# Performance work log

Measured on AMD Instinct MI355X. Metric: run time of the kernel, lower is better.

## Reference

```python
import jax, jax.numpy as jnp
import numpy as np
from jax import lax

DIM = 256          # C
D_INNER = 512      # expand * dim
D_STATE = 16       # N
DT_RANK = 32       # ceil(d_inner / 16)
K_CONV = 4


def setup_inputs() -> dict:
    key = jax.random.key(0)
    ks = jax.random.split(key, 20)
    B, C, H, W = 2, DIM, 64, 64
    Di, N, R = D_INNER, D_STATE, DT_RANK
    s = 0.02
    inp = {
        "decoder_feat": jax.random.normal(ks[0], (B, C, H, W), jnp.float32),
        "encoder_feat": jax.random.normal(ks[1], (B, C, H, W), jnp.float32),
        # CrossMambaFusion params
        "dec_w": jax.random.normal(ks[2], (C, 2 * Di), jnp.float32) * s,
        "dec_b": jnp.zeros((2 * Di,), jnp.float32),
        "enc_w": jax.random.normal(ks[3], (C, Di), jnp.float32) * s,
        "enc_b": jnp.zeros((Di,), jnp.float32),
        "out_w": jax.random.normal(ks[4], (Di, C), jnp.float32) * s,
        "out_b": jnp.zeros((C,), jnp.float32),
        "ln_g": jnp.ones((C,), jnp.float32),
        "ln_b": jnp.zeros((C,), jnp.float32),
        # Mamba block params (inner dim = Di, expand=1.0)
        "in_w": jax.random.normal(ks[5], (Di, 2 * Di), jnp.float32) * s,
        "in_b": jnp.zeros((2 * Di,), jnp.float32),
        "conv_w": jax.random.normal(ks[6], (Di, 1, K_CONV), jnp.float32) * 0.1,
        "conv_b": jnp.zeros((Di,), jnp.float32),
        "x_proj_w": jax.random.normal(ks[7], (Di, R + 2 * N), jnp.float32) * s,
        "dt_w": jax.random.normal(ks[8], (R, Di), jnp.float32) * 0.1,
        "dt_b": jax.random.uniform(ks[9], (Di,), jnp.float32, -4.0, -2.0),  # small dt after softplus
        "A_log": jnp.log(jnp.tile(jnp.arange(1, N + 1, dtype=jnp.float32)[None, :], (Di, 1))),
        "D_param": jnp.ones((Di,), jnp.float32),
        "m_out_w": jax.random.normal(ks[10], (Di, Di), jnp.float32) * s,
        "m_out_b": jnp.zeros((Di,), jnp.float32),
    }
    return inp


def _mamba(x, in_w, in_b, conv_w, conv_b, x_proj_w, dt_w, dt_b, A_log, D_param, m_out_w, m_out_b):
    # x: (B, L, Di)
    Bsz, L, Di = x.shape
    N, R = D_STATE, DT_RANK
    xz = x @ in_w + in_b                      # (B, L, 2*Di)
    xm, z = jnp.split(xz, 2, axis=-1)
    # causal depthwise conv over the sequence axis
    xc = jnp.swapaxes(xm, 1, 2)               # (B, Di, L)
    xc = lax.conv_general_dilated(
        xc, conv_w, window_strides=(1,), padding=[(K_CONV - 1, 0)],
        dimension_numbers=("NCH", "OIH", "NCH"), feature_group_count=Di)
    xc = xc + conv_b[None, :, None]
    u = jax.nn.silu(jnp.swapaxes(xc, 1, 2))   # (B, L, Di)
    x_dbl = u @ x_proj_w                      # (B, L, R+2N)
    dt = jax.nn.softplus(x_dbl[..., :R] @ dt_w + dt_b)   # (B, L, Di)
    Bm = x_dbl[..., R:R + N]                  # (B, L, N)
    Cm = x_dbl[..., R + N:]                   # (B, L, N)
    A = -jnp.exp(A_log)                       # (Di, N)

    def step(h, t):
        dt_t, u_t, B_t, C_t = t               # (B,Di),(B,Di),(B,N),(B,N)
        dA = jnp.exp(dt_t[..., None] * A)     # (B, Di, N)
        h = h * dA + (dt_t * u_t)[..., None] * B_t[:, None, :]
        y = jnp.einsum("bdn,bn->bd", h, C_t)
        return h, y

    h0 = jnp.zeros((Bsz, Di, N), x.dtype)
    _, ys = lax.scan(step, h0, (jnp.swapaxes(dt, 0, 1), jnp.swapaxes(u, 0, 1),
                                jnp.swapaxes(Bm, 0, 1), jnp.swapaxes(Cm, 0, 1)))
    y = jnp.swapaxes(ys, 0, 1) + u * D_param  # skip connection via D
    y = y * jax.nn.silu(z)
    return y @ m_out_w + m_out_b


def reference(decoder_feat, encoder_feat, dec_w, dec_b, enc_w, enc_b, out_w, out_b,
              ln_g, ln_b, in_w, in_b, conv_w, conv_b, x_proj_w, dt_w, dt_b,
              A_log, D_param, m_out_w, m_out_b):
    B, C, H, W = decoder_feat.shape
    Di = D_INNER
    dec = jnp.transpose(decoder_feat, (0, 2, 3, 1)).reshape(B, H * W, C)
    enc = jnp.transpose(encoder_feat, (0, 2, 3, 1)).reshape(B, H * W, C)
    dec_proj = dec @ dec_w + dec_b
    dec_x, dec_gate = dec_proj[..., :Di], dec_proj[..., Di:]
    enc_p = enc @ enc_w + enc_b
    combined = dec_x * jax.nn.sigmoid(enc_p) + enc_p          # (B, L, Di)
    processed = _mamba(combined, in_w, in_b, conv_w, conv_b, x_proj_w,
                       dt_w, dt_b, A_log, D_param, m_out_w, m_out_b)
    out = (processed * jax.nn.sigmoid(dec_gate)) @ out_w + out_b
    res = out + dec
    mu = jnp.mean(res, axis=-1, keepdims=True)
    var = jnp.mean(jnp.square(res - mu), axis=-1, keepdims=True)
    res = (res - mu) * lax.rsqrt(var + 1e-5) * ln_g + ln_b
    return jnp.transpose(res.reshape(B, H, W, C), (0, 3, 1, 2))
```

## Files before the change

### kernel.cpp

```cpp
#include <hip/hip_runtime.h>
#include <hip/hip_bf16.h>

typedef __bf16 bf16x8_t __attribute__((ext_vector_type(8)));
typedef float f32x4_t __attribute__((ext_vector_type(4)));

__device__ __forceinline__ float sigmoidf_(float x) { return 1.0f / (1.0f + __expf(-x)); }
__device__ __forceinline__ float siluf_(float x) { return x * sigmoidf_(x); }
__device__ __forceinline__ float softplusf_(float x) {
    return fmaxf(x, 0.0f) + log1pf(__expf(-fabsf(x)));
}
__device__ __forceinline__ float b2f(ushort u) { return __uint_as_float(((unsigned)u) << 16); }
__device__ __forceinline__ ushort f2b(float f) {
    return (ushort)__bfloat16_as_ushort(__float2bfloat16(f));
}

__global__ __launch_bounds__(256) void k_prep(
    const float* __restrict__ dec_w, const float* __restrict__ enc_w,
    const float* __restrict__ in_w, const float* __restrict__ m_out_w,
    const float* __restrict__ out_w, const float* __restrict__ x_proj_w,
    const float* __restrict__ dt_w,
    const float* __restrict__ dec, const float* __restrict__ enc,
    __hip_bfloat16* __restrict__ dec_wT, __hip_bfloat16* __restrict__ enc_wT,
    __hip_bfloat16* __restrict__ in_wT, __hip_bfloat16* __restrict__ m_out_wT,
    __hip_bfloat16* __restrict__ out_wT, __hip_bfloat16* __restrict__ xpwT,
    __hip_bfloat16* __restrict__ dtwT,
    __hip_bfloat16* __restrict__ decL, __hip_bfloat16* __restrict__ encL)
{
    __shared__ float tile[64][65];
    if (blockIdx.x < 5312) {
        int gid = blockIdx.x * 256 + threadIdx.x;
        const float* src; __hip_bfloat16* dst; int lk, N, idx;
        if (gid < 262144)       { src = dec_w;    dst = dec_wT;   lk = 8; N = 1024; idx = gid; }
        else if (gid < 393216)  { src = enc_w;    dst = enc_wT;   lk = 8; N = 512;  idx = gid - 262144; }
        else if (gid < 917504)  { src = in_w;     dst = in_wT;    lk = 9; N = 1024; idx = gid - 393216; }
        else if (gid < 1179648) { src = m_out_w;  dst = m_out_wT; lk = 9; N = 512;  idx = gid - 917504; }
        else if (gid < 1310720) { src = out_w;    dst = out_wT;   lk = 9; N = 256;  idx = gid - 1179648; }
        else if (gid < 1343488) { src = x_proj_w; dst = xpwT;     lk = 9; N = 64;   idx = gid - 1310720; }
        else                    { src = dt_w;     dst = dtwT;     lk = 5; N = 512;  idx = gid - 1343488; }
        int K = 1 << lk;
        int n = idx >> lk, k = idx & (K - 1);
        dst[idx] = __float2bfloat16(src[(size_t)k * N + n]);
        return;
    }
    const int bid = blockIdx.x - 5312;
    const int t = threadIdx.x;
    const int ct = bid & 3;
    const int lt = (bid >> 2) & 63;
    const int sel = bid >> 8;
    const int b = sel & 1, ten = sel >> 1;
    const float* src = ten ? enc : dec;
    __hip_bfloat16* dst = ten ? encL : decL;
    const size_t ibase = (size_t)b * 256 * 4096 + (size_t)(ct * 64) * 4096 + (size_t)lt * 64;
#pragma unroll
    for (int i = 0; i < 16; ++i) {
        int c = i * 4 + (t >> 6), l = t & 63;
        tile[c][l] = src[ibase + (size_t)c * 4096 + l];
    }
    __syncthreads();
    const size_t obase = ((size_t)b * 4096 + (size_t)lt * 64) * 256 + ct * 64;
#pragma unroll
    for (int i = 0; i < 16; ++i) {
        int l = i * 4 + (t >> 6), c = t & 63;
        dst[obase + (size_t)l * 256 + c] = __float2bfloat16(tile[c][l]);
    }
}

template <int EPI, int K>
__global__ __launch_bounds__(256) void bgemm(
    const __hip_bfloat16* __restrict__ A, const __hip_bfloat16* __restrict__ Bt,
    const float* __restrict__ bias, void* __restrict__ out0,
    void* __restrict__ out1, const void* __restrict__ extra)
{
    __shared__ ushort At[128 * 32];
    __shared__ ushort Bl[128 * 32];
    const int tid = threadIdx.x;
    const int wave = tid >> 6, lane = tid & 63;
    const int n0 = blockIdx.x * 128, m0 = blockIdx.y * 128;
    const int wm = (wave >> 1) * 64, wn = (wave & 1) * 64;
    f32x4_t acc[4][4] = {};
    const int fr = lane & 15, fq = (lane >> 4) * 8;

    for (int k0 = 0; k0 < K; k0 += 32) {
#pragma unroll
        for (int q = 0; q < 2; ++q) {
            int idx = q * 256 + tid;
            int row = idx >> 2, ch = (idx & 3) * 8;
            uint4 va = *(const uint4*)&A[(size_t)(m0 + row) * K + k0 + ch];
            uint4 vb = *(const uint4*)&Bt[(size_t)(n0 + row) * K + k0 + ch];
            *(uint4*)&At[row * 32 + ch] = va;
            *(uint4*)&Bl[row * 32 + ch] = vb;
        }
        __syncthreads();
        bf16x8_t af[4], bf[4];
#pragma unroll
        for (int i = 0; i < 4; ++i) {
            af[i] = *(bf16x8_t*)&At[(wm + i * 16 + fr) * 32 + fq];
            bf[i] = *(bf16x8_t*)&Bl[(wn + i * 16 + fr) * 32 + fq];
        }
#pragma unroll
        for (int i = 0; i < 4; ++i)
#pragma unroll
            for (int j = 0; j < 4; ++j)
                acc[i][j] = __builtin_amdgcn_mfma_f32_16x16x32_bf16(af[i], bf[j], acc[i][j], 0, 0, 0);
        __syncthreads();
    }

    const int col = lane & 15, rbase = (lane >> 4) * 4;
#pragma unroll
    for (int i = 0; i < 4; ++i) {
#pragma unroll
        for (int j = 0; j < 4; ++j) {
#pragma unroll
            for (int r = 0; r < 4; ++r) {
                int m = m0 + wm + i * 16 + rbase + r;
                int n = n0 + wn + j * 16 + col;
                float v = acc[i][j][r] + bias[n];
                if (EPI == 0) {
                    ((__hip_bfloat16*)out0)[(size_t)m * 512 + n] = __float2bfloat16(v);
                } else if (EPI == 1) {
                    if (n < 512) {
                        float ep = __bfloat162float(((const __hip_bfloat16*)extra)[(size_t)m * 512 + n]);
                        ((__hip_bfloat16*)out0)[(size_t)m * 512 + n] =
                            __float2bfloat16(fmaf(v, sigmoidf_(ep), ep));
                    } else {
                        ((__hip_bfloat16*)out1)[(size_t)m * 512 + (n - 512)] =
                            __float2bfloat16(sigmoidf_(v));
                    }
                } else if (EPI == 2) {
                    if (n < 512)
                        ((__hip_bfloat16*)out0)[(size_t)m * 512 + n] = __float2bfloat16(v);
                    else
                        ((__hip_bfloat16*)out1)[(size_t)m * 512 + (n - 512)] =
                            __float2bfloat16(siluf_(v));
                } else {
                    float g = __bfloat162float(((const __hip_bfloat16*)extra)[(size_t)m * 512 + n]);
                    ((__hip_bfloat16*)out0)[(size_t)m * 512 + n] = __float2bfloat16(v * g);
                }
            }
        }
    }
}

#define CHUNK 16
#define NCHUNK 256

__global__ __launch_bounds__(512) void k_conv_scan(
    const __hip_bfloat16* __restrict__ xm, const float* __restrict__ conv_w,
    const float* __restrict__ conv_b, const __hip_bfloat16* __restrict__ xpwT,
    const __hip_bfloat16* __restrict__ dtwT, const float* __restrict__ dt_b,
    const float* __restrict__ A_log,
    __hip_bfloat16* __restrict__ u_out, float* __restrict__ Bm,
    float* __restrict__ Cm, __hip_bfloat16* __restrict__ dt_out,
    ushort* __restrict__ hpart, float* __restrict__ dtsums)
{
    __shared__ __align__(16) ushort us_dts[CHUNK][512 + 8];
    __shared__ __align__(16) ushort adt[CHUNK][32 + 8];
    __shared__ float BsL[CHUNK * 16];
    const int tid = threadIdx.x;
    const int wave = tid >> 6, lane = tid & 63;
    const int bl0 = blockIdx.x * CHUNK;
    const int l0 = bl0 & 4095;
    const int b = blockIdx.x >> 8;
    const int chunk = blockIdx.x & (NCHUNK - 1);
    const int fr = lane & 15, fq = (lane >> 4) * 8;
    const int col = lane & 15, rbase = (lane >> 4) * 4;

    float uarr[CHUNK];
    {
        const int d = tid;
        const float cw0 = conv_w[d * 4], cw1 = conv_w[d * 4 + 1];
        const float cw2 = conv_w[d * 4 + 2], cw3 = conv_w[d * 4 + 3];
        const float cb = conv_b[d];
        const ushort* xs = (const ushort*)xm;
        float x0 = (l0 >= 3) ? b2f(xs[(size_t)(bl0 - 3) * 512 + d]) : 0.f;
        float x1 = (l0 >= 2) ? b2f(xs[(size_t)(bl0 - 2) * 512 + d]) : 0.f;
        float x2 = (l0 >= 1) ? b2f(xs[(size_t)(bl0 - 1) * 512 + d]) : 0.f;
#pragma unroll
        for (int t = 0; t < CHUNK; ++t) {
            float x3 = b2f(xs[(size_t)(bl0 + t) * 512 + d]);
            float a = cb;
            a = fmaf(cw0, x0, a);
            a = fmaf(cw1, x1, a);
            a = fmaf(cw2, x2, a);
            a = fmaf(cw3, x3, a);
            float uv = siluf_(a);
            uarr[t] = uv;
            ushort ub = f2b(uv);
            us_dts[t][d] = ub;
            ((ushort*)u_out)[(size_t)(bl0 + t) * 512 + d] = ub;
            x0 = x1; x1 = x2; x2 = x3;
        }
    }
    __syncthreads();

    if (wave < 4) {
        const int n0w = wave * 16;
        f32x4_t acc = {};
        const __hip_bfloat16* bp = xpwT + (size_t)(n0w + fr) * 512;
#pragma unroll
        for (int k0 = 0; k0 < 512; k0 += 32) {
            bf16x8_t af = *(bf16x8_t*)&us_dts[fr][k0 + fq];
            bf16x8_t bf = *(const bf16x8_t*)&bp[k0 + fq];
            acc = __builtin_amdgcn_mfma_f32_16x16x32_bf16(af, bf, acc, 0, 0, 0);
        }
#pragma unroll
        for (int r = 0; r < 4; ++r) {
            int m = rbase + r;
            int n = n0w + col;
            float v = acc[r];
            if (n < 32) {
                adt[m][n] = f2b(v);
            } else if (n < 48) {
                BsL[m * 16 + (n - 32)] = v;
                Bm[(size_t)(bl0 + m) * 16 + (n - 32)] = v;
            } else {
                Cm[(size_t)(bl0 + m) * 16 + (n - 48)] = v;
            }
        }
    }
    __syncthreads();

    {
        bf16x8_t af = *(bf16x8_t*)&adt[fr][fq];
#pragma unroll
        for (int t = 0; t < 4; ++t) {
            int nt = wave * 4 + t;
            bf16x8_t bf = *(const bf16x8_t*)&dtwT[(size_t)(nt * 16 + fr) * 32 + fq];
            f32x4_t acc = {};
            acc = __builtin_amdgcn_mfma_f32_16x16x32_bf16(af, bf, acc, 0, 0, 0);
#pragma unroll
            for (int r = 0; r < 4; ++r) {
                int m = rbase + r;
                int n = nt * 16 + col;
                ushort dv = f2b(softplusf_(acc[r] + dt_b[n]));
                us_dts[m][n] = dv;
                ((ushort*)dt_out)[(size_t)(bl0 + m) * 512 + n] = dv;
            }
        }
    }
    __syncthreads();

    {
        const int d = tid;
        float Av[16];
#pragma unroll
        for (int n = 0; n < 16; n += 4) {
            float4 al = *(const float4*)&A_log[d * 16 + n];
            Av[n + 0] = -__expf(al.x);
            Av[n + 1] = -__expf(al.y);
            Av[n + 2] = -__expf(al.z);
            Av[n + 3] = -__expf(al.w);
        }
        float h[16] = {};
        float dtsum = 0.f;
#pragma unroll
        for (int t = 0; t < CHUNK; ++t) {
            float dtv = b2f(us_dts[t][d]);
            float dtu = dtv * uarr[t];
            dtsum += dtv;
            const float* Bt = &BsL[t * 16];
#pragma unroll
            for (int n = 0; n < 16; ++n)
                h[n] = fmaf(h[n], __expf(dtv * Av[n]), dtu * Bt[n]);
        }
        const size_t sidx = ((size_t)b * NCHUNK + chunk) * 512 + d;
        const size_t idx = sidx * 16;
        ushort hb[16];
#pragma unroll
        for (int n = 0; n < 16; ++n) hb[n] = f2b(h[n]);
        *(uint4*)&hpart[idx]     = *(uint4*)&hb[0];
        *(uint4*)&hpart[idx + 8] = *(uint4*)&hb[8];
        dtsums[sidx] = dtsum;
    }
}

__global__ __launch_bounds__(64) void k_scan_comb(
    const ushort* __restrict__ hpart, const float* __restrict__ dtsums,
    const float* __restrict__ A_log, ushort* __restrict__ h_in)
{
    const int gid = blockIdx.x * 64 + threadIdx.x;
    const int n = gid & 15;
    const int d = (gid >> 4) & 511;
    const int b = gid >> 13;
    const float Av = -__expf(A_log[d * 16 + n]);
    float h = 0.f;
    for (int c = 0; c < NCHUNK; ++c) {
        const size_t sidx = ((size_t)b * NCHUNK + c) * 512 + d;
        const size_t idx = sidx * 16 + n;
        h_in[idx] = f2b(h);
        h = fmaf(h, __expf(Av * dtsums[sidx]), b2f(hpart[idx]));
    }
}

__global__ __launch_bounds__(512) void k_scan_fin(
    const __hip_bfloat16* __restrict__ dt, const __hip_bfloat16* __restrict__ u,
    const float* __restrict__ Bmp, const float* __restrict__ Cmp,
    const float* __restrict__ A_log, const float* __restrict__ Dp,
    const __hip_bfloat16* __restrict__ zs, const ushort* __restrict__ h_in,
    __hip_bfloat16* __restrict__ yout)
{
    __shared__ float Bs[CHUNK * 16];
    __shared__ float Cs[CHUNK * 16];
    const int d = threadIdx.x;
    const int chunk = blockIdx.x & (NCHUNK - 1);
    const int b = blockIdx.x >> 8;
    const size_t row0 = (size_t)b * 4096 + (size_t)chunk * CHUNK;

    if (d < CHUNK * 16) {
        Bs[d] = Bmp[row0 * 16 + d];
        Cs[d] = Cmp[row0 * 16 + d];
    }
    float Av[16];
#pragma unroll
    for (int n = 0; n < 16; n += 4) {
        float4 al = *(const float4*)&A_log[d * 16 + n];
        Av[n + 0] = -__expf(al.x);
        Av[n + 1] = -__expf(al.y);
        Av[n + 2] = -__expf(al.z);
        Av[n + 3] = -__expf(al.w);
    }
    const float Dv = Dp[d];
    float h[16];
    {
        const size_t idx = (((size_t)b * NCHUNK + chunk) * 512 + d) * 16;
        ushort hb[16];
        *(uint4*)&hb[0] = *(const uint4*)&h_in[idx];
        *(uint4*)&hb[8] = *(const uint4*)&h_in[idx + 8];
#pragma unroll
        for (int n = 0; n < 16; ++n) h[n] = b2f(hb[n]);
    }
    __syncthreads();

    const ushort* dtp = (const ushort*)dt + row0 * 512 + d;
    const ushort* up = (const ushort*)u + row0 * 512 + d;
    const ushort* zp = (const ushort*)zs + row0 * 512 + d;
    __hip_bfloat16* yp = yout + row0 * 512 + d;
#pragma unroll
    for (int t = 0; t < CHUNK; ++t) {
        float dtv = b2f(dtp[(size_t)t * 512]);
        float uv = b2f(up[(size_t)t * 512]);
        float zv = b2f(zp[(size_t)t * 512]);
        float dtu = dtv * uv;
        const float* Bt = &Bs[t * 16];
        const float* Ct = &Cs[t * 16];
        float y = 0.f;
#pragma unroll
        for (int n = 0; n < 16; ++n) {
            h[n] = fmaf(h[n], __expf(dtv * Av[n]), dtu * Bt[n]);
            y = fmaf(h[n], Ct[n], y);
        }
        yp[(size_t)t * 512] = __float2bfloat16((y + uv * Dv) * zv);
    }
}

__global__ __launch_bounds__(256) void k_out_ln(
    const __hip_bfloat16* __restrict__ A, const __hip_bfloat16* __restrict__ Bt,
    const float* __restrict__ bias, const __hip_bfloat16* __restrict__ decL,
    const float* __restrict__ ln_g, const float* __restrict__ ln_b,
    float* __restrict__ outp)
{
    __shared__ ushort At[32 * 32];
    __shared__ ushort Bl[256 * 32];
    __shared__ float red[4][32][2];
    __shared__ float lmu[32], lsc[32];
    const int tid = threadIdx.x;
    const int wave = tid >> 6, lane = tid & 63;
    const int m0 = blockIdx.x * 32;
    const int wn = wave * 64;
    f32x4_t acc[2][4] = {};
    const int fr = lane & 15, fq = (lane >> 4) * 8;

    for (int k0 = 0; k0 < 512; k0 += 32) {
        if (tid < 128) {
            int row = tid >> 2, ch = (tid & 3) * 8;
            *(uint4*)&At[row * 32 + ch] = *(const uint4*)&A[(size_t)(m0 + row) * 512 + k0 + ch];
        }
#pragma unroll
        for (int q = 0; q < 4; ++q) {
            int idx = q * 256 + tid;
            int row = idx >> 2, ch = (idx & 3) * 8;
            *(uint4*)&Bl[row * 32 + ch] = *(const uint4*)&Bt[(size_t)row * 512 + k0 + ch];
        }
        __syncthreads();
        bf16x8_t af[2], bf[4];
#pragma unroll
        for (int i = 0; i < 2; ++i)
            af[i] = *(bf16x8_t*)&At[(i * 16 + fr) * 32 + fq];
#pragma unroll
        for (int j = 0; j < 4; ++j)
            bf[j] = *(bf16x8_t*)&Bl[(wn + j * 16 + fr) * 32 + fq];
#pragma unroll
        for (int i = 0; i < 2; ++i)
#pragma unroll
            for (int j = 0; j < 4; ++j)
                acc[i][j] = __builtin_amdgcn_mfma_f32_16x16x32_bf16(af[i], bf[j], acc[i][j], 0, 0, 0);
        __syncthreads();
    }

    const int col = lane & 15, rbase = (lane >> 4) * 4;
#pragma unroll
    for (int i = 0; i < 2; ++i) {
#pragma unroll
        for (int r = 0; r < 4; ++r) {
            int ml = i * 16 + rbase + r;
            int m = m0 + ml;
            float s = 0.f, sq = 0.f;
#pragma unroll
            for (int j = 0; j < 4; ++j) {
                int n = wn + j * 16 + col;
                float dv = b2f(((const ushort*)decL)[(size_t)m * 256 + n]);
                float v = acc[i][j][r] + bias[n] + dv;
                acc[i][j][r] = v;
                s += v;
                sq = fmaf(v, v, sq);
            }
            s += __shfl_xor(s, 1);  sq += __shfl_xor(sq, 1);
            s += __shfl_xor(s, 2);  sq += __shfl_xor(sq, 2);
            s += __shfl_xor(s, 4);  sq += __shfl_xor(sq, 4);
            s += __shfl_xor(s, 8);  sq += __shfl_xor(sq, 8);
            if (col == 0) { red[wave][ml][0] = s; red[wave][ml][1] = sq; }
        }
    }
    __syncthreads();
    if (tid < 32) {
        float s  = red[0][tid][0] + red[1][tid][0] + red[2][tid][0] + red[3][tid][0];
        float sq = red[0][tid][1] + red[1][tid][1] + red[2][tid][1] + red[3][tid][1];
        float mu = s * (1.0f / 256.0f);
        float var = sq * (1.0f / 256.0f) - mu * mu;
        lmu[tid] = mu;
        lsc[tid] = rsqrtf(var + 1e-5f);
    }
    __syncthreads();
    const int bb = m0 >> 12;
    const int lpos0 = m0 & 4095;
#pragma unroll
    for (int i = 0; i < 2; ++i) {
#pragma unroll
        for (int r = 0; r < 4; ++r) {
            int ml = i * 16 + rbase + r;
            float mu = lmu[ml], sc = lsc[ml];
#pragma unroll
            for (int j = 0; j < 4; ++j) {
                int n = wn + j * 16 + col;
                float v = (acc[i][j][r] - mu) * sc * ln_g[n] + ln_b[n];
                outp[(size_t)bb * (256 * 4096) + (size_t)n * 4096 + lpos0 + ml] = v;
            }
        }
    }
}

extern "C" void kernel_launch(void* const* d_in, const int* in_sizes, int n_in,
                              void* d_out, int out_size, void* d_ws, size_t ws_size,
                              hipStream_t stream)
{
    const float* decoder_feat = (const float*)d_in[0];
    const float* encoder_feat = (const float*)d_in[1];
    const float* dec_w = (const float*)d_in[2];
    const float* dec_b = (const float*)d_in[3];
    const float* enc_w = (const float*)d_in[4];
    const float* enc_b = (const float*)d_in[5];
    const float* out_w = (const float*)d_in[6];
    const float* out_b = (const float*)d_in[7];
    const float* ln_g = (const float*)d_in[8];
    const float* ln_bb = (const float*)d_in[9];
    const float* in_w = (const float*)d_in[10];
    const float* in_b = (const float*)d_in[11];
    const float* conv_w = (const float*)d_in[12];
    const float* conv_b = (const float*)d_in[13];
    const float* x_proj_w = (const float*)d_in[14];
    const float* dt_w = (const float*)d_in[15];
    const float* dt_b = (const float*)d_in[16];
    const float* A_log = (const float*)d_in[17];
    const float* D_param = (const float*)d_in[18];
    const float* m_out_w = (const float*)d_in[19];
    const float* m_out_b = (const float*)d_in[20];

    float* outp = (float*)d_out;
    char* ws = (char*)d_ws;
    const size_t MB = 1024ull * 1024;
    __hip_bfloat16* decL     = (__hip_bfloat16*)(ws + 0 * MB);
    __hip_bfloat16* encL     = (__hip_bfloat16*)(ws + 4 * MB);
    __hip_bfloat16* dec_wT   = (__hip_bfloat16*)(ws + 8 * MB);
    __hip_bfloat16* enc_wT   = (__hip_bfloat16*)(ws + 9 * MB);
    __hip_bfloat16* in_wT    = (__hip_bfloat16*)(ws + 10 * MB);
    __hip_bfloat16* m_out_wT = (__hip_bfloat16*)(ws + 11 * MB);
    __hip_bfloat16* out_wT   = (__hip_bfloat16*)(ws + 12 * MB);
    __hip_bfloat16* xpwT     = (__hip_bfloat16*)(ws + 12 * MB + 262144);
    __hip_bfloat16* dtwT     = (__hip_bfloat16*)(ws + 12 * MB + 262144 + 65536);
    __hip_bfloat16* enc_pb   = (__hip_bfloat16*)(ws + 13 * MB);
    __hip_bfloat16* combined = (__hip_bfloat16*)(ws + 29 * MB);
    __hip_bfloat16* gate_sig = (__hip_bfloat16*)(ws + 37 * MB);
    __hip_bfloat16* xm       = (__hip_bfloat16*)(ws + 45 * MB);
    __hip_bfloat16* z_silu   = (__hip_bfloat16*)(ws + 53 * MB);
    __hip_bfloat16* u_buf    = (__hip_bfloat16*)(ws + 61 * MB);
    __hip_bfloat16* dt_buf   = (__hip_bfloat16*)(ws + 69 * MB);
    ushort* h_in             = (ushort*)(ws + 77 * MB);
    float* Bm                = (float*)(ws + 93 * MB);
    float* Cm                = (float*)(ws + 93 * MB + 524288);
    float* dtsums            = (float*)(ws + 94 * MB);
    ushort* hpart = (ushort*)(ws + 13 * MB);
    __hip_bfloat16* y_buf = combined;
    __hip_bfloat16* gated = xm;

    k_prep<<<6336, 256, 0, stream>>>(
        dec_w, enc_w, in_w, m_out_w, out_w, x_proj_w, dt_w,
        decoder_feat, encoder_feat,
        dec_wT, enc_wT, in_wT, m_out_wT, out_wT, xpwT, dtwT, decL, encL);
    bgemm<0, 256><<<dim3(4, 64), 256, 0, stream>>>(
        encL, enc_wT, enc_b, enc_pb, nullptr, nullptr);
    bgemm<1, 256><<<dim3(8, 64), 256, 0, stream>>>(
        decL, dec_wT, dec_b, combined, gate_sig, enc_pb);
    bgemm<2, 512><<<dim3(8, 64), 256, 0, stream>>>(
        combined, in_wT, in_b, xm, z_silu, nullptr);
    k_conv_scan<<<2 * NCHUNK, 512, 0, stream>>>(
        xm, conv_w, conv_b, xpwT, dtwT, dt_b, A_log,
        u_buf, Bm, Cm, dt_buf, hpart, dtsums);
    k_scan_comb<<<256, 64, 0, stream>>>(hpart, dtsums, A_log, h_in);
    k_scan_fin<<<2 * NCHUNK, 512, 0, stream>>>(
        dt_buf, u_buf, Bm, Cm, A_log, D_param, z_silu, h_in, y_buf);
    bgemm<3, 512><<<dim3(4, 64), 256, 0, stream>>>(
        y_buf, m_out_wT, m_out_b, gated, nullptr, gate_sig);
    k_out_ln<<<256, 256, 0, stream>>>(
        gated, out_wT, out_b, decL, ln_g, ln_bb, outp);
}
```

Baseline: 283.7 us.

## Fuse Mamba output projection, gating, out-projection and LayerNorm into one tail kernel

Replaces the separate m_out GEMM (with sigmoid-gate epilogue) and the out-projection+LayerNorm kernel with a single 512-thread kernel. Each block keeps its 32 rows in LDS, computes the first GEMM, writes the gated bf16 result back into the LDS tile, then runs the second GEMM and LayerNorm. Weight B operands are read directly from global memory instead of being staged through LDS. The NCHW output store is transposed through LDS so that each thread writes contiguous runs. This removes one launch and the round trip of the gated intermediate through global memory. In exchange, every block reads both full weight matrices from global/L2 with no LDS reuse.

```diff
diff --git a/kernel.cpp b/kernel.cpp
--- a/kernel.cpp
+++ b/kernel.cpp
@@ -126,15 +126,12 @@
                         ((__hip_bfloat16*)out1)[(size_t)m * 512 + (n - 512)] =
                             __float2bfloat16(sigmoidf_(v));
                     }
-                } else if (EPI == 2) {
+                } else {
                     if (n < 512)
                         ((__hip_bfloat16*)out0)[(size_t)m * 512 + n] = __float2bfloat16(v);
                     else
                         ((__hip_bfloat16*)out1)[(size_t)m * 512 + (n - 512)] =
                             __float2bfloat16(siluf_(v));
-                } else {
-                    float g = __bfloat162float(((const __hip_bfloat16*)extra)[(size_t)m * 512 + n]);
-                    ((__hip_bfloat16*)out0)[(size_t)m * 512 + n] = __float2bfloat16(v * g);
                 }
             }
         }
@@ -353,73 +350,99 @@
     }
 }
 
-__global__ __launch_bounds__(256) void k_out_ln(
-    const __hip_bfloat16* __restrict__ A, const __hip_bfloat16* __restrict__ Bt,
-    const float* __restrict__ bias, const __hip_bfloat16* __restrict__ decL,
+__global__ __launch_bounds__(512) void k_tail(
+    const __hip_bfloat16* __restrict__ y, const __hip_bfloat16* __restrict__ m_out_wT,
+    const float* __restrict__ m_out_b, const __hip_bfloat16* __restrict__ gate_sig,
+    const __hip_bfloat16* __restrict__ out_wT, const float* __restrict__ out_b,
+    const __hip_bfloat16* __restrict__ decL,
     const float* __restrict__ ln_g, const float* __restrict__ ln_b,
     float* __restrict__ outp)
 {
-    __shared__ ushort At[32 * 32];
-    __shared__ ushort Bl[256 * 32];
-    __shared__ float red[4][32][2];
-    __shared__ float lmu[32], lsc[32];
+    __shared__ __align__(16) char smem[32 * 520 * 2 + 1024 + 256];
+    ushort (*tile)[520] = (ushort(*)[520])smem;
+    float (*lt)[257] = (float(*)[257])smem;
+    float (*red)[32][2] = (float(*)[32][2])(smem + 33280);
+    float* lmu = (float*)(smem + 33280 + 1024);
+    float* lsc = lmu + 32;
+
     const int tid = threadIdx.x;
     const int wave = tid >> 6, lane = tid & 63;
     const int m0 = blockIdx.x * 32;
-    const int wn = wave * 64;
-    f32x4_t acc[2][4] = {};
     const int fr = lane & 15, fq = (lane >> 4) * 8;
-
+    const int col = lane & 15, rbase = (lane >> 4) * 4;
+
+    {
+        int row = tid >> 4, ch = (tid & 15) * 32;
+        const ushort* src = (const ushort*)y + (size_t)(m0 + row) * 512 + ch;
+#pragma unroll
+        for (int q = 0; q < 4; ++q)
+            *(uint4*)&tile[row][ch + q * 8] = *(const uint4*)&src[q * 8];
+    }
+    __syncthreads();
+
+    const int wn1 = wave * 64;
+    f32x4_t acc1[2][4] = {};
+#pragma unroll
     for (int k0 = 0; k0 < 512; k0 += 32) {
-        if (tid < 128) {
-            int row = tid >> 2, ch = (tid & 3) * 8;
-            *(uint4*)&At[row * 32 + ch] = *(const uint4*)&A[(size_t)(m0 + row) * 512 + k0 + ch];
-        }
-#pragma unroll
-        for (int q = 0; q < 4; ++q) {
-            int idx = q * 256 + tid;
-            int row = idx >> 2, ch = (idx & 3) * 8;
-            *(uint4*)&Bl[row * 32 + ch] = *(const uint4*)&Bt[(size_t)row * 512 + k0 + ch];
-        }
-        __syncthreads();
         bf16x8_t af[2], bf[4];
 #pragma unroll
         for (int i = 0; i < 2; ++i)
-            af[i] = *(bf16x8_t*)&At[(i * 16 + fr) * 32 + fq];
+            af[i] = *(bf16x8_t*)&tile[i * 16 + fr][k0 + fq];
 #pragma unroll
         for (int j = 0; j < 4; ++j)
-            bf[j] = *(bf16x8_t*)&Bl[(wn + j * 16 + fr) * 32 + fq];
+            bf[j] = *(const bf16x8_t*)&m_out_wT[(size_t)(wn1 + j * 16 + fr) * 512 + k0 + fq];
 #pragma unroll
         for (int i = 0; i < 2; ++i)
 #pragma unroll
             for (int j = 0; j < 4; ++j)
-                acc[i][j] = __builtin_amdgcn_mfma_f32_16x16x32_bf16(af[i], bf[j], acc[i][j], 0, 0, 0);
-        __syncthreads();
-    }
-
-    const int col = lane & 15, rbase = (lane >> 4) * 4;
-#pragma unroll
-    for (int i = 0; i < 2; ++i) {
-#pragma unroll
-        for (int r = 0; r < 4; ++r) {
-            int ml = i * 16 + rbase + r;
-            int m = m0 + ml;
-            float s = 0.f, sq = 0.f;
-#pragma unroll
-            for (int j = 0; j < 4; ++j) {
-                int n = wn + j * 16 + col;
-                float dv = b2f(((const ushort*)decL)[(size_t)m * 256 + n]);
-                float v = acc[i][j][r] + bias[n] + dv;
-                acc[i][j][r] = v;
-                s += v;
-                sq = fmaf(v, v, sq);
+                acc1[i][j] = __builtin_amdgcn_mfma_f32_16x16x32_bf16(af[i], bf[j], acc1[i][j], 0, 0, 0);
+    }
+    __syncthreads();
+
+#pragma unroll
+    for (int i = 0; i < 2; ++i)
+#pragma unroll
+        for (int j = 0; j < 4; ++j)
+#pragma unroll
+            for (int r = 0; r < 4; ++r) {
+                int ml = i * 16 + rbase + r;
+                int n = wn1 + j * 16 + col;
+                float g = b2f(((const ushort*)gate_sig)[(size_t)(m0 + ml) * 512 + n]);
+                tile[ml][n] = f2b((acc1[i][j][r] + m_out_b[n]) * g);
             }
-            s += __shfl_xor(s, 1);  sq += __shfl_xor(sq, 1);
-            s += __shfl_xor(s, 2);  sq += __shfl_xor(sq, 2);
-            s += __shfl_xor(s, 4);  sq += __shfl_xor(sq, 4);
-            s += __shfl_xor(s, 8);  sq += __shfl_xor(sq, 8);
-            if (col == 0) { red[wave][ml][0] = s; red[wave][ml][1] = sq; }
-        }
+    __syncthreads();
+
+    const int mh = wave >> 2, wn2 = (wave & 3) * 64;
+    f32x4_t acc2[4] = {};
+#pragma unroll
+    for (int k0 = 0; k0 < 512; k0 += 32) {
+        bf16x8_t af = *(bf16x8_t*)&tile[mh * 16 + fr][k0 + fq];
+#pragma unroll
+        for (int j = 0; j < 4; ++j) {
+            bf16x8_t bf = *(const bf16x8_t*)&out_wT[(size_t)(wn2 + j * 16 + fr) * 512 + k0 + fq];
+            acc2[j] = __builtin_amdgcn_mfma_f32_16x16x32_bf16(af, bf, acc2[j], 0, 0, 0);
+        }
+    }
+
+#pragma unroll
+    for (int r = 0; r < 4; ++r) {
+        int ml = mh * 16 + rbase + r;
+        int m = m0 + ml;
+        float s = 0.f, sq = 0.f;
+#pragma unroll
+        for (int j = 0; j < 4; ++j) {
+            int n = wn2 + j * 16 + col;
+            float dv = b2f(((const ushort*)decL)[(size_t)m * 256 + n]);
+            float v = acc2[j][r] + out_b[n] + dv;
+            acc2[j][r] = v;
+            s += v;
+            sq = fmaf(v, v, sq);
+        }
+        s += __shfl_xor(s, 1);  sq += __shfl_xor(sq, 1);
+        s += __shfl_xor(s, 2);  sq += __shfl_xor(sq, 2);
+        s += __shfl_xor(s, 4);  sq += __shfl_xor(sq, 4);
+        s += __shfl_xor(s, 8);  sq += __shfl_xor(sq, 8);
+        if (col == 0) { red[wave & 3][ml][0] = s; red[wave & 3][ml][1] = sq; }
     }
     __syncthreads();
     if (tid < 32) {
@@ -431,21 +454,27 @@
         lsc[tid] = rsqrtf(var + 1e-5f);
     }
     __syncthreads();
-    const int bb = m0 >> 12;
-    const int lpos0 = m0 & 4095;
-#pragma unroll
-    for (int i = 0; i < 2; ++i) {
-#pragma unroll
-        for (int r = 0; r < 4; ++r) {
-            int ml = i * 16 + rbase + r;
-            float mu = lmu[ml], sc = lsc[ml];
-#pragma unroll
-            for (int j = 0; j < 4; ++j) {
-                int n = wn + j * 16 + col;
-                float v = (acc[i][j][r] - mu) * sc * ln_g[n] + ln_b[n];
-                outp[(size_t)bb * (256 * 4096) + (size_t)n * 4096 + lpos0 + ml] = v;
-            }
-        }
+
+#pragma unroll
+    for (int r = 0; r < 4; ++r) {
+        int ml = mh * 16 + rbase + r;
+        float mu = lmu[ml], sc = lsc[ml];
+#pragma unroll
+        for (int j = 0; j < 4; ++j) {
+            int n = wn2 + j * 16 + col;
+            lt[ml][n] = (acc2[j][r] - mu) * sc * ln_g[n] + ln_b[n];
+        }
+    }
+    __syncthreads();
+
+    {
+        const int bb = m0 >> 12;
+        const int lpos0 = m0 & 4095;
+        int c = tid >> 1, half = (tid & 1) * 16;
+        float* dst = outp + (size_t)bb * (256 * 4096) + (size_t)c * 4096 + lpos0 + half;
+#pragma unroll
+        for (int s = 0; s < 16; ++s)
+            dst[s] = lt[half + s][c];
     }
 }
 
@@ -500,7 +529,6 @@
     float* dtsums            = (float*)(ws + 94 * MB);
     ushort* hpart = (ushort*)(ws + 13 * MB);
     __hip_bfloat16* y_buf = combined;
-    __hip_bfloat16* gated = xm;
 
     k_prep<<<6336, 256, 0, stream>>>(
         dec_w, enc_w, in_w, m_out_w, out_w, x_proj_w, dt_w,
@@ -518,8 +546,7 @@
     k_scan_comb<<<256, 64, 0, stream>>>(hpart, dtsums, A_log, h_in);
     k_scan_fin<<<2 * NCHUNK, 512, 0, stream>>>(
         dt_buf, u_buf, Bm, Cm, A_log, D_param, z_silu, h_in, y_buf);
-    bgemm<3, 512><<<dim3(4, 64), 256, 0, stream>>>(
-        y_buf, m_out_wT, m_out_b, gated, nullptr, gate_sig);
-    k_out_ln<<<256, 256, 0, stream>>>(
-        gated, out_wT, out_b, decL, ln_g, ln_bb, outp);
-}
+    k_tail<<<256, 512, 0, stream>>>(
+        y_buf, m_out_wT, m_out_b, gate_sig, out_wT, out_b, decL,
+        ln_g, ln_bb, outp);
+}
```

Measured after the change: 293.7 us. 3.6% more time.
